# Kernel tuning notes

Measured on AMD Instinct MI355X. Metric: run time of the kernel, lower is better.

## Reference

```python
import math
import jax, jax.numpy as jnp
import numpy as np

B, N, E, H = 1, 4096, 256, 8
D = E // H  # head dim = 32


def setup_inputs() -> dict:
    key = jax.random.key(0)
    ks = jax.random.split(key, 10)
    s = 1.0 / math.sqrt(E)
    return {
        "x": jax.random.normal(ks[0], (B, N, E), dtype=jnp.float32),
        "adjacency": jax.random.randint(ks[1], (B, N, N), 0, 2, dtype=jnp.int32),
        "Wq": jax.random.normal(ks[2], (E, E), dtype=jnp.float32) * s,
        "bq": jnp.zeros((E,), dtype=jnp.float32),
        "Wk": jax.random.normal(ks[3], (E, E), dtype=jnp.float32) * s,
        "bk": jnp.zeros((E,), dtype=jnp.float32),
        "Wv": jax.random.normal(ks[4], (E, E), dtype=jnp.float32) * s,
        "bv": jnp.zeros((E,), dtype=jnp.float32),
        "Wo": jax.random.normal(ks[5], (E, E), dtype=jnp.float32) * s,
        "bo": jnp.zeros((E,), dtype=jnp.float32),
    }


def reference(x, adjacency, Wq, bq, Wk, bk, Wv, bv, Wo, bo):
    b, n, e = x.shape
    # projections (torch Linear: x @ W.T + b), split into heads -> [B,H,N,D]
    def heads(y):
        return y.reshape(b, n, H, D).transpose(0, 2, 1, 3)
    q = heads(x @ Wq.T + bq)
    k = heads(x @ Wk.T + bk)
    v = heads(x @ Wv.T + bv)
    scores = jnp.einsum("bhnd,bhmd->bhnm", q, k) / math.sqrt(D)
    mask = (adjacency[:, None, :, :] == 0)  # [B,1,N,N]
    scores = jnp.where(mask, -jnp.inf, scores)
    w = jax.nn.softmax(scores, axis=-1)
    out = jnp.einsum("bhnm,bhmd->bhnd", w, v)
    out = out.transpose(0, 2, 1, 3).reshape(b, n, e)
    return out @ Wo.T + bo
```

## Files before the change

### kernel.cpp

```cpp
#include <hip/hip_runtime.h>
#include <math.h>


#define NTOK 4096
#define EDIM 256
#define HEADS 8
#define HD 32
#define NSPLIT 2
#define QSCALE 0.17677669529663687f
#define LOG2E 1.4426950408889634f
#define CINIT (-11.541560327111707f)

typedef __attribute__((ext_vector_type(8))) short bf16x8;
typedef __attribute__((ext_vector_type(4))) float f32x4;
typedef __attribute__((ext_vector_type(4))) unsigned long long u64x4;

static __device__ inline short f2bf(float f) {
    unsigned u = __float_as_uint(f);
    u = (u + 0x7FFFu + ((u >> 16) & 1u)) >> 16;
    return (short)u;
}
static __device__ inline unsigned packtrunc(float a, float b) {
    return __builtin_amdgcn_perm(__float_as_uint(b), __float_as_uint(a),
                                 0x07060302u);
}
static __device__ inline float sel_mask(float v, unsigned long long m) {
    float r;
    asm("v_cndmask_b32 %0, 0, %1, %2" : "=v"(r) : "v"(v), "s"(m));
    return r;
}

__global__ __launch_bounds__(256) void prep(
    const int* __restrict__ adj, unsigned long long* __restrict__ maskT,
    const float* __restrict__ x,  const float* __restrict__ Wq,
    const float* __restrict__ Wk, const float* __restrict__ Wv,
    const float* __restrict__ Wo,
    short* __restrict__ xb,  short* __restrict__ wqb,
    short* __restrict__ wkb, short* __restrict__ wvb,
    short* __restrict__ wob)
{
    const int bid = blockIdx.x;
    if (bid < 16384) {
        const int w = bid * 4 + (threadIdx.x >> 6);
        const int l = threadIdx.x & 63;
        const int qb = w >> 8;
        const int kt = (w >> 2) & 63;
        const int b = w & 3;
        const int row = qb * 16 + (l & 15);
        const int col = kt * 64 + b * 16 + ((l >> 4) & 3) * 4;
        const int4 av = *(const int4*)&adj[row * NTOK + col];
        const unsigned long long m0 = __ballot(av.x != 0);
        const unsigned long long m1 = __ballot(av.y != 0);
        const unsigned long long m2 = __ballot(av.z != 0);
        const unsigned long long m3 = __ballot(av.w != 0);
        if (l == 0) {
            unsigned long long* dst = &maskT[(size_t)w * 4];
            dst[0] = m0; dst[1] = m1; dst[2] = m2; dst[3] = m3;
        }
    } else {
        const int gid = (bid - 16384) * 256 + threadIdx.x;
        const int e = gid * 4;
        const float* src; short* dst; int off;
        if (e < NTOK * EDIM) { src = x; dst = xb; off = e; }
        else {
            const int r = e - NTOK * EDIM;
            const int wsel = r >> 16;
            off = r & 65535;
            src = (wsel == 0) ? Wq : (wsel == 1) ? Wk : (wsel == 2) ? Wv : Wo;
            dst = (wsel == 0) ? wqb : (wsel == 1) ? wkb : (wsel == 2) ? wvb : wob;
        }
        float4 v = *(const float4*)&src[off];
        uint2 t;
        t.x = (unsigned short)f2bf(v.x) | ((unsigned)(unsigned short)f2bf(v.y) << 16);
        t.y = (unsigned short)f2bf(v.z) | ((unsigned)(unsigned short)f2bf(v.w) << 16);
        *(uint2*)&dst[off] = t;
    }
}

__global__ __launch_bounds__(256) void qkv_mfma(
    const short* __restrict__ xb,
    const short* __restrict__ Wqb, const short* __restrict__ Wkb,
    const short* __restrict__ Wvb,
    const float* __restrict__ bq, const float* __restrict__ bk,
    const float* __restrict__ bv,
    short* __restrict__ qo, short* __restrict__ ko, short* __restrict__ vto)
{
    const int tid = threadIdx.x;
    const int wv = tid >> 6, lane = tid & 63;
    const int grp = lane >> 4, lcol = lane & 15;
    const int wsel = blockIdx.y >> 2;
    const int n0 = (blockIdx.y & 3) << 6;
    const int m0 = blockIdx.x * 64 + wv * 16;
    const short* __restrict__ W = (wsel == 0) ? Wqb : (wsel == 1) ? Wkb : Wvb;
    const float* __restrict__ bias = (wsel == 0) ? bq : (wsel == 1) ? bk : bv;

    bf16x8 af[8];
#pragma unroll
    for (int k = 0; k < 8; ++k)
        af[k] = *(const bf16x8*)&xb[(m0 + lcol) * 256 + k * 32 + grp * 8];

    f32x4 acc[4] = {};
#pragma unroll
    for (int k = 0; k < 8; ++k) {
#pragma unroll
        for (int t = 0; t < 4; ++t) {
            const bf16x8 bt =
                *(const bf16x8*)&W[(n0 + t * 16 + lcol) * 256 + k * 32 + grp * 8];
            acc[t] = __builtin_amdgcn_mfma_f32_16x16x32_bf16(af[k], bt, acc[t], 0, 0, 0);
        }
    }
#pragma unroll
    for (int t = 0; t < 4; ++t) {
        const int feat = n0 + t * 16 + lcol;
        const float bval = bias[feat];
        const int h = feat >> 5, d = feat & 31;
        if (wsel == 2) {
            uint2 o;
            o.x = (unsigned short)f2bf(acc[t][0] + bval) |
                  ((unsigned)(unsigned short)f2bf(acc[t][1] + bval) << 16);
            o.y = (unsigned short)f2bf(acc[t][2] + bval) |
                  ((unsigned)(unsigned short)f2bf(acc[t][3] + bval) << 16);
            *(uint2*)&vto[h * (HD * NTOK) + d * NTOK + m0 + grp * 4] = o;
        } else {
            short* __restrict__ out = (wsel == 0) ? qo : ko;
            const float sc = (wsel == 0) ? (QSCALE * LOG2E) : 1.0f;
#pragma unroll
            for (int j = 0; j < 4; ++j)
                out[h * (NTOK * HD) + (m0 + grp * 4 + j) * HD + d] =
                    f2bf((acc[t][j] + bval) * sc);
        }
    }
}

__global__ __launch_bounds__(256) void attn_mfma(
    const short* __restrict__ qg, const short* __restrict__ kg,
    const short* __restrict__ vtg, const unsigned long long* __restrict__ maskT,
    float* __restrict__ o_part, float* __restrict__ l_part)
{
    const int h = blockIdx.y;
    const int split = blockIdx.z;
    const int q0 = blockIdx.x << 6;
    const short* __restrict__ Q  = qg  + h * (NTOK * HD);
    const short* __restrict__ K  = kg  + h * (NTOK * HD);
    const short* __restrict__ Vt = vtg + h * (HD * NTOK);

    __shared__ short Ks[2][64][40];
    __shared__ short Vs[2][32][72];
    __shared__ short P_lds[4][16][76];

    const int tid = threadIdx.x;
    const int wv = tid >> 6;
    const int lane = tid & 63;
    const int grp = lane >> 4;
    const int lcol = lane & 15;
    const int q0w = q0 + wv * 16;

    const int krow = tid >> 2, kc8 = (tid & 3) << 3;
    const int vrow = tid >> 3, vc8 = (tid & 7) << 3;

    const bf16x8 qfrag = *(const bf16x8*)&Q[(q0w + lcol) * HD + grp * 8];

    const int qb = __builtin_amdgcn_readfirstlane(blockIdx.x * 4 + wv);
    const unsigned long long* __restrict__ mbase = maskT + (size_t)qb * 1024;

    f32x4 ot[2] = {};
    float lsum = 0.f;

    const int kt_begin = split * (64 / NSPLIT);
    const int kt_end = kt_begin + (64 / NSPLIT);

    {
        const int k0 = kt_begin << 6;
        const int4 kr = *(const int4*)&K[(k0 + krow) * HD + kc8];
        const int4 vr = *(const int4*)&Vt[vrow * NTOK + k0 + vc8];
        *(int4*)&Ks[0][krow][kc8] = kr;
        *(int4*)&Vs[0][vrow][vc8] = vr;
    }
    __syncthreads();

    int cur = 0;
    for (int kt = kt_begin; kt < kt_end; ++kt) {
        int4 kr, vr;
        const bool has_next = (kt + 1 < kt_end);
        if (has_next) {
            const int k0n = (kt + 1) << 6;
            kr = *(const int4*)&K[(k0n + krow) * HD + kc8];
            vr = *(const int4*)&Vt[vrow * NTOK + k0n + vc8];
        }

        const u64x4* mp = (const u64x4*)(mbase + kt * 16);
        const u64x4 wa = mp[0], wb = mp[1], wc = mp[2], wd = mp[3];

        bf16x8 kf[4], vf[4];
#pragma unroll
        for (int b = 0; b < 4; ++b)
            kf[b] = *(const bf16x8*)&Ks[cur][b * 16 + lcol][grp * 8];
#pragma unroll
        for (int c = 0; c < 2; ++c) {
            vf[c * 2 + 0] = *(const bf16x8*)&Vs[cur][c * 16 + lcol][grp * 8];
            vf[c * 2 + 1] = *(const bf16x8*)&Vs[cur][c * 16 + lcol][32 + grp * 8];
        }

        f32x4 s[4];
#pragma unroll
        for (int b = 0; b < 4; ++b)
            s[b] = __builtin_amdgcn_mfma_f32_16x16x32_bf16(
                kf[b], qfrag, (f32x4){CINIT, CINIT, CINIT, CINIT}, 0, 0, 0);

#pragma unroll
        for (int b = 0; b < 4; ++b) {
            const u64x4 wj = (b == 0) ? wa : (b == 1) ? wb : (b == 2) ? wc : wd;
            const float p0 = sel_mask(__builtin_amdgcn_exp2f(s[b][0]), wj[0]);
            const float p1 = sel_mask(__builtin_amdgcn_exp2f(s[b][1]), wj[1]);
            const float p2 = sel_mask(__builtin_amdgcn_exp2f(s[b][2]), wj[2]);
            const float p3 = sel_mask(__builtin_amdgcn_exp2f(s[b][3]), wj[3]);
            lsum += (p0 + p1) + (p2 + p3);
            uint2 t;
            t.x = packtrunc(p0, p1);
            t.y = packtrunc(p2, p3);
            *(uint2*)&P_lds[wv][lcol][b * 16 + grp * 4] = t;
        }

        const uint2 pl0 = *(const uint2*)&P_lds[wv][lcol][grp * 8];
        const uint2 pl1 = *(const uint2*)&P_lds[wv][lcol][grp * 8 + 4];
        const uint2 pl2 = *(const uint2*)&P_lds[wv][lcol][32 + grp * 8];
        const uint2 pl3 = *(const uint2*)&P_lds[wv][lcol][32 + grp * 8 + 4];
        struct { uint2 a, b; } u0 = {pl0, pl1}, u1 = {pl2, pl3};
        const bf16x8 pf0 = __builtin_bit_cast(bf16x8, u0);
        const bf16x8 pf1 = __builtin_bit_cast(bf16x8, u1);

#pragma unroll
        for (int c = 0; c < 2; ++c) {
            ot[c] = __builtin_amdgcn_mfma_f32_16x16x32_bf16(vf[c * 2 + 0], pf0, ot[c], 0, 0, 0);
            ot[c] = __builtin_amdgcn_mfma_f32_16x16x32_bf16(vf[c * 2 + 1], pf1, ot[c], 0, 0, 0);
        }

        if (has_next) {
            *(int4*)&Ks[cur ^ 1][krow][kc8] = kr;
            *(int4*)&Vs[cur ^ 1][vrow][vc8] = vr;
        }
        __syncthreads();
        cur ^= 1;
    }

    lsum += __shfl_xor(lsum, 16);
    lsum += __shfl_xor(lsum, 32);

    float* __restrict__ ob = o_part + split * (NTOK * EDIM);
#pragma unroll
    for (int c = 0; c < 2; ++c) {
        float4 st;
        st.x = ot[c][0]; st.y = ot[c][1]; st.z = ot[c][2]; st.w = ot[c][3];
        *(float4*)&ob[(q0w + lcol) * EDIM + h * HD + c * 16 + grp * 4] = st;
    }
    if (grp == 0)
        l_part[split * (NTOK * HEADS) + (q0w + lcol) * HEADS + h] = lsum;
}

__global__ __launch_bounds__(256) void out_mfma(
    const float* __restrict__ o_part, const float* __restrict__ l_part,
    const short* __restrict__ Wob, const float* __restrict__ bo,
    float* __restrict__ Y)
{
    const int tid = threadIdx.x;
    const int wv = tid >> 6, lane = tid & 63;
    const int grp = lane >> 4, lcol = lane & 15;
    const int n0 = blockIdx.y << 6;
    const int m0 = blockIdx.x * 64 + wv * 16;
    const int r = m0 + lcol;

    bf16x8 af[8];
#pragma unroll
    for (int k = 0; k < 8; ++k) {
        float4 s0 = {0.f, 0.f, 0.f, 0.f}, s1 = {0.f, 0.f, 0.f, 0.f};
        float lv = 0.f;
#pragma unroll
        for (int s = 0; s < NSPLIT; ++s) {
            const float* op = &o_part[s * (NTOK * EDIM) + r * EDIM + k * 32 + grp * 8];
            const float4 t0 = *(const float4*)op;
            const float4 t1 = *(const float4*)(op + 4);
            s0.x += t0.x; s0.y += t0.y; s0.z += t0.z; s0.w += t0.w;
            s1.x += t1.x; s1.y += t1.y; s1.z += t1.z; s1.w += t1.w;
            lv += l_part[s * (NTOK * HEADS) + r * HEADS + k];
        }
        const float inv = 1.0f / lv;
        bf16x8 t;
        t[0] = f2bf(s0.x * inv); t[1] = f2bf(s0.y * inv);
        t[2] = f2bf(s0.z * inv); t[3] = f2bf(s0.w * inv);
        t[4] = f2bf(s1.x * inv); t[5] = f2bf(s1.y * inv);
        t[6] = f2bf(s1.z * inv); t[7] = f2bf(s1.w * inv);
        af[k] = t;
    }

    f32x4 acc[4] = {};
#pragma unroll
    for (int k = 0; k < 8; ++k) {
#pragma unroll
        for (int t = 0; t < 4; ++t) {
            const bf16x8 bt =
                *(const bf16x8*)&Wob[(n0 + t * 16 + lcol) * 256 + k * 32 + grp * 8];
            acc[t] = __builtin_amdgcn_mfma_f32_16x16x32_bf16(af[k], bt, acc[t], 0, 0, 0);
        }
    }
#pragma unroll
    for (int t = 0; t < 4; ++t) {
        const float bval = bo[n0 + t * 16 + lcol];
#pragma unroll
        for (int j = 0; j < 4; ++j)
            Y[(m0 + grp * 4 + j) * EDIM + n0 + t * 16 + lcol] = acc[t][j] + bval;
    }
}

extern "C" void kernel_launch(void* const* d_in, const int* in_sizes, int n_in,
                              void* d_out, int out_size, void* d_ws, size_t ws_size,
                              hipStream_t stream) {
    (void)in_sizes; (void)n_in; (void)out_size; (void)ws_size;
    const float* x  = (const float*)d_in[0];
    const int*  adj = (const int*)d_in[1];
    const float* Wq = (const float*)d_in[2];
    const float* bq = (const float*)d_in[3];
    const float* Wk = (const float*)d_in[4];
    const float* bk = (const float*)d_in[5];
    const float* Wv = (const float*)d_in[6];
    const float* bv = (const float*)d_in[7];
    const float* Wo = (const float*)d_in[8];
    const float* bo = (const float*)d_in[9];

    char* ws = (char*)d_ws;
    short* x_bf  = (short*)(ws);
    short* q_ws  = (short*)(ws + (2u << 20));
    short* k_ws  = (short*)(ws + (4u << 20));
    short* vt_ws = (short*)(ws + (6u << 20));
    unsigned long long* maskT =
        (unsigned long long*)(ws + (8u << 20));
    short* Wq_bf = (short*)(ws + (10u << 20));
    short* Wk_bf = Wq_bf + (EDIM * EDIM);
    short* Wv_bf = Wk_bf + (EDIM * EDIM);
    short* Wo_bf = Wv_bf + (EDIM * EDIM);
    float* l_part = (float*)(ws + (11u << 20));
    float* o_part = (float*)(ws + (12u << 20));

    prep<<<dim3(16384 + 1280), 256, 0, stream>>>(
        adj, maskT, x, Wq, Wk, Wv, Wo, x_bf, Wq_bf, Wk_bf, Wv_bf, Wo_bf);
    qkv_mfma<<<dim3(64, 12), 256, 0, stream>>>(x_bf, Wq_bf, Wk_bf, Wv_bf,
                                               bq, bk, bv, q_ws, k_ws, vt_ws);
    attn_mfma<<<dim3(64, HEADS, NSPLIT), 256, 0, stream>>>(
        q_ws, k_ws, vt_ws, maskT, o_part, l_part);
    out_mfma<<<dim3(64, 4), 256, 0, stream>>>(o_part, l_part, Wo_bf, bo,
                                              (float*)d_out);
}
```

Baseline: 179.3 us.

## Load K/V fragments directly from global into registers, compute row sums via MFMA

Removes the shared-memory K/V staging and per-tile __syncthreads, so each wave loads its MFMA fragments straight from global memory into registers with a two-tile register double buffer. The softmax denominator is now accumulated with extra MFMAs against a ones vector instead of scalar adds plus cross-lane shuffles. s_setprio hints are wrapped around the MFMA groups. In exchange, the four waves in a block now each fetch the same K/V data separately, relying on cache, and register pressure goes up.

```diff
diff --git a/kernel.cpp b/kernel.cpp
--- a/kernel.cpp
+++ b/kernel.cpp
@@ -144,8 +144,6 @@
     const short* __restrict__ K  = kg  + h * (NTOK * HD);
     const short* __restrict__ Vt = vtg + h * (HD * NTOK);
 
-    __shared__ short Ks[2][64][40];
-    __shared__ short Vs[2][32][72];
     __shared__ short P_lds[4][16][76];
 
     const int tid = threadIdx.x;
@@ -155,96 +153,90 @@
     const int lcol = lane & 15;
     const int q0w = q0 + wv * 16;
 
-    const int krow = tid >> 2, kc8 = (tid & 3) << 3;
-    const int vrow = tid >> 3, vc8 = (tid & 7) << 3;
-
     const bf16x8 qfrag = *(const bf16x8*)&Q[(q0w + lcol) * HD + grp * 8];
 
     const int qb = __builtin_amdgcn_readfirstlane(blockIdx.x * 4 + wv);
     const unsigned long long* __restrict__ mbase = maskT + (size_t)qb * 1024;
 
     f32x4 ot[2] = {};
-    float lsum = 0.f;
-
-    const int kt_begin = split * (64 / NSPLIT);
-    const int kt_end = kt_begin + (64 / NSPLIT);
-
-    {
-        const int k0 = kt_begin << 6;
-        const int4 kr = *(const int4*)&K[(k0 + krow) * HD + kc8];
-        const int4 vr = *(const int4*)&Vt[vrow * NTOK + k0 + vc8];
-        *(int4*)&Ks[0][krow][kc8] = kr;
-        *(int4*)&Vs[0][vrow][vc8] = vr;
-    }
-    __syncthreads();
-
-    int cur = 0;
-    for (int kt = kt_begin; kt < kt_end; ++kt) {
-        int4 kr, vr;
-        const bool has_next = (kt + 1 < kt_end);
-        if (has_next) {
-            const int k0n = (kt + 1) << 6;
-            kr = *(const int4*)&K[(k0n + krow) * HD + kc8];
-            vr = *(const int4*)&Vt[vrow * NTOK + k0n + vc8];
-        }
-
-        const u64x4* mp = (const u64x4*)(mbase + kt * 16);
-        const u64x4 wa = mp[0], wb = mp[1], wc = mp[2], wd = mp[3];
-
-        bf16x8 kf[4], vf[4];
-#pragma unroll
-        for (int b = 0; b < 4; ++b)
-            kf[b] = *(const bf16x8*)&Ks[cur][b * 16 + lcol][grp * 8];
-#pragma unroll
-        for (int c = 0; c < 2; ++c) {
-            vf[c * 2 + 0] = *(const bf16x8*)&Vs[cur][c * 16 + lcol][grp * 8];
-            vf[c * 2 + 1] = *(const bf16x8*)&Vs[cur][c * 16 + lcol][32 + grp * 8];
-        }
-
-        f32x4 s[4];
-#pragma unroll
-        for (int b = 0; b < 4; ++b)
-            s[b] = __builtin_amdgcn_mfma_f32_16x16x32_bf16(
-                kf[b], qfrag, (f32x4){CINIT, CINIT, CINIT, CINIT}, 0, 0, 0);
-
-#pragma unroll
-        for (int b = 0; b < 4; ++b) {
-            const u64x4 wj = (b == 0) ? wa : (b == 1) ? wb : (b == 2) ? wc : wd;
-            const float p0 = sel_mask(__builtin_amdgcn_exp2f(s[b][0]), wj[0]);
-            const float p1 = sel_mask(__builtin_amdgcn_exp2f(s[b][1]), wj[1]);
-            const float p2 = sel_mask(__builtin_amdgcn_exp2f(s[b][2]), wj[2]);
-            const float p3 = sel_mask(__builtin_amdgcn_exp2f(s[b][3]), wj[3]);
-            lsum += (p0 + p1) + (p2 + p3);
-            uint2 t;
-            t.x = packtrunc(p0, p1);
-            t.y = packtrunc(p2, p3);
-            *(uint2*)&P_lds[wv][lcol][b * 16 + grp * 4] = t;
-        }
-
-        const uint2 pl0 = *(const uint2*)&P_lds[wv][lcol][grp * 8];
-        const uint2 pl1 = *(const uint2*)&P_lds[wv][lcol][grp * 8 + 4];
-        const uint2 pl2 = *(const uint2*)&P_lds[wv][lcol][32 + grp * 8];
-        const uint2 pl3 = *(const uint2*)&P_lds[wv][lcol][32 + grp * 8 + 4];
-        struct { uint2 a, b; } u0 = {pl0, pl1}, u1 = {pl2, pl3};
-        const bf16x8 pf0 = __builtin_bit_cast(bf16x8, u0);
-        const bf16x8 pf1 = __builtin_bit_cast(bf16x8, u1);
-
-#pragma unroll
-        for (int c = 0; c < 2; ++c) {
-            ot[c] = __builtin_amdgcn_mfma_f32_16x16x32_bf16(vf[c * 2 + 0], pf0, ot[c], 0, 0, 0);
-            ot[c] = __builtin_amdgcn_mfma_f32_16x16x32_bf16(vf[c * 2 + 1], pf1, ot[c], 0, 0, 0);
-        }
-
-        if (has_next) {
-            *(int4*)&Ks[cur ^ 1][krow][kc8] = kr;
-            *(int4*)&Vs[cur ^ 1][vrow][vc8] = vr;
-        }
-        __syncthreads();
-        cur ^= 1;
-    }
-
-    lsum += __shfl_xor(lsum, 16);
-    lsum += __shfl_xor(lsum, 32);
+    f32x4 lacc = {};
+    const f32x4 cinit = {CINIT, CINIT, CINIT, CINIT};
+    bf16x8 ones;
+#pragma unroll
+    for (int i = 0; i < 8; ++i) ones[i] = (short)0x3F80;
+
+    const int NT = 64 / NSPLIT;
+    const int kt_begin = split * NT;
+
+    const short* __restrict__ kp = &K[(kt_begin * 64 + lcol) * HD + grp * 8];
+    const short* __restrict__ vp = &Vt[lcol * NTOK + kt_begin * 64 + grp * 8];
+
+#define LOADKV(KF, VF, T)                                                   \
+    {                                                                       \
+        const short* kpp = kp + (T) * (64 * HD);                            \
+        const short* vpp = vp + (T) * 64;                                   \
+        KF[0] = *(const bf16x8*)(kpp);                                      \
+        KF[1] = *(const bf16x8*)(kpp + 16 * HD);                            \
+        KF[2] = *(const bf16x8*)(kpp + 32 * HD);                            \
+        KF[3] = *(const bf16x8*)(kpp + 48 * HD);                            \
+        VF[0] = *(const bf16x8*)(vpp);                                      \
+        VF[1] = *(const bf16x8*)(vpp + 32);                                 \
+        VF[2] = *(const bf16x8*)(vpp + 16 * NTOK);                          \
+        VF[3] = *(const bf16x8*)(vpp + 16 * NTOK + 32);                     \
+    }
+
+#define TILE(KF, VF, KT)                                                    \
+    {                                                                       \
+        const u64x4* mp = (const u64x4*)(mbase + (size_t)(KT) * 16);        \
+        const u64x4 wa = mp[0], wb = mp[1], wcm = mp[2], wdm = mp[3];       \
+        f32x4 s[4];                                                         \
+        __builtin_amdgcn_s_setprio(1);                                      \
+        _Pragma("unroll")                                                   \
+        for (int b = 0; b < 4; ++b)                                         \
+            s[b] = __builtin_amdgcn_mfma_f32_16x16x32_bf16(                 \
+                KF[b], qfrag, cinit, 0, 0, 0);                              \
+        __builtin_amdgcn_s_setprio(0);                                      \
+        _Pragma("unroll")                                                   \
+        for (int b = 0; b < 4; ++b) {                                       \
+            const u64x4 wj = (b == 0) ? wa : (b == 1) ? wb                  \
+                             : (b == 2) ? wcm : wdm;                        \
+            const float p0 = sel_mask(__builtin_amdgcn_exp2f(s[b][0]), wj[0]); \
+            const float p1 = sel_mask(__builtin_amdgcn_exp2f(s[b][1]), wj[1]); \
+            const float p2 = sel_mask(__builtin_amdgcn_exp2f(s[b][2]), wj[2]); \
+            const float p3 = sel_mask(__builtin_amdgcn_exp2f(s[b][3]), wj[3]); \
+            uint2 t;                                                        \
+            t.x = packtrunc(p0, p1);                                        \
+            t.y = packtrunc(p2, p3);                                        \
+            *(uint2*)&P_lds[wv][lcol][b * 16 + grp * 4] = t;                \
+        }                                                                   \
+        const uint2 pl0 = *(const uint2*)&P_lds[wv][lcol][grp * 8];         \
+        const uint2 pl1 = *(const uint2*)&P_lds[wv][lcol][grp * 8 + 4];     \
+        const uint2 pl2 = *(const uint2*)&P_lds[wv][lcol][32 + grp * 8];    \
+        const uint2 pl3 = *(const uint2*)&P_lds[wv][lcol][32 + grp * 8 + 4];\
+        struct { uint2 a, b; } u0 = {pl0, pl1}, u1 = {pl2, pl3};            \
+        const bf16x8 pf0 = __builtin_bit_cast(bf16x8, u0);                  \
+        const bf16x8 pf1 = __builtin_bit_cast(bf16x8, u1);                  \
+        __builtin_amdgcn_s_setprio(1);                                      \
+        ot[0] = __builtin_amdgcn_mfma_f32_16x16x32_bf16(VF[0], pf0, ot[0], 0, 0, 0); \
+        ot[0] = __builtin_amdgcn_mfma_f32_16x16x32_bf16(VF[1], pf1, ot[0], 0, 0, 0); \
+        ot[1] = __builtin_amdgcn_mfma_f32_16x16x32_bf16(VF[2], pf0, ot[1], 0, 0, 0); \
+        ot[1] = __builtin_amdgcn_mfma_f32_16x16x32_bf16(VF[3], pf1, ot[1], 0, 0, 0); \
+        lacc  = __builtin_amdgcn_mfma_f32_16x16x32_bf16(ones,  pf0, lacc, 0, 0, 0);  \
+        lacc  = __builtin_amdgcn_mfma_f32_16x16x32_bf16(ones,  pf1, lacc, 0, 0, 0);  \
+        __builtin_amdgcn_s_setprio(0);                                      \
+    }
+
+    bf16x8 kA[4], vA[4], kB[4], vB[4];
+    LOADKV(kA, vA, 0)
+#pragma unroll 1
+    for (int t = 0; t < NT; t += 2) {
+        LOADKV(kB, vB, t + 1)
+        TILE(kA, vA, kt_begin + t)
+        if (t + 2 < NT) LOADKV(kA, vA, t + 2)
+        TILE(kB, vB, kt_begin + t + 1)
+    }
+#undef LOADKV
+#undef TILE
 
     float* __restrict__ ob = o_part + split * (NTOK * EDIM);
 #pragma unroll
@@ -254,7 +246,7 @@
         *(float4*)&ob[(q0w + lcol) * EDIM + h * HD + c * 16 + grp * 4] = st;
     }
     if (grp == 0)
-        l_part[split * (NTOK * HEADS) + (q0w + lcol) * HEADS + h] = lsum;
+        l_part[split * (NTOK * HEADS) + (q0w + lcol) * HEADS + h] = lacc[0];
 }
 
 __global__ __launch_bounds__(256) void out_mfma(
```

Result: slower. 226.2 us (+26.2%).

## Split attention over four key chunks, compute row sums via MFMA, regrid output GEMM

Applied to the files above, without the earlier changes.

The attention kernel now takes its key-split count from the grid (4 when the workspace is large enough, otherwise 2), doubling the number of blocks to improve occupancy across CUs. The softmax denominator is accumulated with an extra MFMA against a ones vector instead of scalar adds and shuffles, and MFMA sections get raised wave priority. The output projection is regridded so each wave computes one 16x16 tile, giving 4x more blocks, and it reduces a runtime number of partials. The cost is extra partial-buffer traffic and reduction work, plus the row sum now comes from bf16-truncated P.

```diff
diff --git a/kernel.cpp b/kernel.cpp
--- a/kernel.cpp
+++ b/kernel.cpp
@@ -6,7 +6,6 @@
 #define EDIM 256
 #define HEADS 8
 #define HD 32
-#define NSPLIT 2
 #define QSCALE 0.17677669529663687f
 #define LOG2E 1.4426950408889634f
 #define CINIT (-11.541560327111707f)
@@ -164,10 +163,15 @@
     const unsigned long long* __restrict__ mbase = maskT + (size_t)qb * 1024;
 
     f32x4 ot[2] = {};
-    float lsum = 0.f;
-
-    const int kt_begin = split * (64 / NSPLIT);
-    const int kt_end = kt_begin + (64 / NSPLIT);
+    f32x4 lacc = {};
+    const f32x4 cinit = {CINIT, CINIT, CINIT, CINIT};
+    bf16x8 ones;
+#pragma unroll
+    for (int i = 0; i < 8; ++i) ones[i] = (short)0x3F80;
+
+    const int tps = 64 / (int)gridDim.z;
+    const int kt_begin = split * tps;
+    const int kt_end = kt_begin + tps;
 
     {
         const int k0 = kt_begin << 6;
@@ -202,10 +206,12 @@
         }
 
         f32x4 s[4];
+        __builtin_amdgcn_s_setprio(1);
 #pragma unroll
         for (int b = 0; b < 4; ++b)
             s[b] = __builtin_amdgcn_mfma_f32_16x16x32_bf16(
-                kf[b], qfrag, (f32x4){CINIT, CINIT, CINIT, CINIT}, 0, 0, 0);
+                kf[b], qfrag, cinit, 0, 0, 0);
+        __builtin_amdgcn_s_setprio(0);
 
 #pragma unroll
         for (int b = 0; b < 4; ++b) {
@@ -214,7 +220,6 @@
             const float p1 = sel_mask(__builtin_amdgcn_exp2f(s[b][1]), wj[1]);
             const float p2 = sel_mask(__builtin_amdgcn_exp2f(s[b][2]), wj[2]);
             const float p3 = sel_mask(__builtin_amdgcn_exp2f(s[b][3]), wj[3]);
-            lsum += (p0 + p1) + (p2 + p3);
             uint2 t;
             t.x = packtrunc(p0, p1);
             t.y = packtrunc(p2, p3);
@@ -229,11 +234,15 @@
         const bf16x8 pf0 = __builtin_bit_cast(bf16x8, u0);
         const bf16x8 pf1 = __builtin_bit_cast(bf16x8, u1);
 
+        __builtin_amdgcn_s_setprio(1);
 #pragma unroll
         for (int c = 0; c < 2; ++c) {
             ot[c] = __builtin_amdgcn_mfma_f32_16x16x32_bf16(vf[c * 2 + 0], pf0, ot[c], 0, 0, 0);
             ot[c] = __builtin_amdgcn_mfma_f32_16x16x32_bf16(vf[c * 2 + 1], pf1, ot[c], 0, 0, 0);
         }
+        lacc = __builtin_amdgcn_mfma_f32_16x16x32_bf16(ones, pf0, lacc, 0, 0, 0);
+        lacc = __builtin_amdgcn_mfma_f32_16x16x32_bf16(ones, pf1, lacc, 0, 0, 0);
+        __builtin_amdgcn_s_setprio(0);
 
         if (has_next) {
             *(int4*)&Ks[cur ^ 1][krow][kc8] = kr;
@@ -242,9 +251,6 @@
         __syncthreads();
         cur ^= 1;
     }
-
-    lsum += __shfl_xor(lsum, 16);
-    lsum += __shfl_xor(lsum, 32);
 
     float* __restrict__ ob = o_part + split * (NTOK * EDIM);
 #pragma unroll
@@ -254,19 +260,19 @@
         *(float4*)&ob[(q0w + lcol) * EDIM + h * HD + c * 16 + grp * 4] = st;
     }
     if (grp == 0)
-        l_part[split * (NTOK * HEADS) + (q0w + lcol) * HEADS + h] = lsum;
+        l_part[split * (NTOK * HEADS) + (q0w + lcol) * HEADS + h] = lacc[0];
 }
 
 __global__ __launch_bounds__(256) void out_mfma(
     const float* __restrict__ o_part, const float* __restrict__ l_part,
     const short* __restrict__ Wob, const float* __restrict__ bo,
-    float* __restrict__ Y)
+    float* __restrict__ Y, int ns)
 {
     const int tid = threadIdx.x;
     const int wv = tid >> 6, lane = tid & 63;
     const int grp = lane >> 4, lcol = lane & 15;
-    const int n0 = blockIdx.y << 6;
-    const int m0 = blockIdx.x * 64 + wv * 16;
+    const int m0 = blockIdx.x << 4;
+    const int n0 = (blockIdx.y << 6) + wv * 16;
     const int r = m0 + lcol;
 
     bf16x8 af[8];
@@ -274,8 +280,7 @@
     for (int k = 0; k < 8; ++k) {
         float4 s0 = {0.f, 0.f, 0.f, 0.f}, s1 = {0.f, 0.f, 0.f, 0.f};
         float lv = 0.f;
-#pragma unroll
-        for (int s = 0; s < NSPLIT; ++s) {
+        for (int s = 0; s < ns; ++s) {
             const float* op = &o_part[s * (NTOK * EDIM) + r * EDIM + k * 32 + grp * 8];
             const float4 t0 = *(const float4*)op;
             const float4 t1 = *(const float4*)(op + 4);
@@ -292,29 +297,23 @@
         af[k] = t;
     }
 
-    f32x4 acc[4] = {};
+    f32x4 acc = {};
 #pragma unroll
     for (int k = 0; k < 8; ++k) {
-#pragma unroll
-        for (int t = 0; t < 4; ++t) {
-            const bf16x8 bt =
-                *(const bf16x8*)&Wob[(n0 + t * 16 + lcol) * 256 + k * 32 + grp * 8];
-            acc[t] = __builtin_amdgcn_mfma_f32_16x16x32_bf16(af[k], bt, acc[t], 0, 0, 0);
-        }
-    }
-#pragma unroll
-    for (int t = 0; t < 4; ++t) {
-        const float bval = bo[n0 + t * 16 + lcol];
-#pragma unroll
-        for (int j = 0; j < 4; ++j)
-            Y[(m0 + grp * 4 + j) * EDIM + n0 + t * 16 + lcol] = acc[t][j] + bval;
-    }
+        const bf16x8 bt =
+            *(const bf16x8*)&Wob[(n0 + lcol) * 256 + k * 32 + grp * 8];
+        acc = __builtin_amdgcn_mfma_f32_16x16x32_bf16(af[k], bt, acc, 0, 0, 0);
+    }
+    const float bval = bo[n0 + lcol];
+#pragma unroll
+    for (int j = 0; j < 4; ++j)
+        Y[(m0 + grp * 4 + j) * EDIM + n0 + lcol] = acc[j] + bval;
 }
 
 extern "C" void kernel_launch(void* const* d_in, const int* in_sizes, int n_in,
                               void* d_out, int out_size, void* d_ws, size_t ws_size,
                               hipStream_t stream) {
-    (void)in_sizes; (void)n_in; (void)out_size; (void)ws_size;
+    (void)in_sizes; (void)n_in; (void)out_size;
     const float* x  = (const float*)d_in[0];
     const int*  adj = (const int*)d_in[1];
     const float* Wq = (const float*)d_in[2];
@@ -340,12 +339,14 @@
     float* l_part = (float*)(ws + (11u << 20));
     float* o_part = (float*)(ws + (12u << 20));
 
+    const int ns = (ws_size >= (28u << 20)) ? 4 : 2;
+
     prep<<<dim3(16384 + 1280), 256, 0, stream>>>(
         adj, maskT, x, Wq, Wk, Wv, Wo, x_bf, Wq_bf, Wk_bf, Wv_bf, Wo_bf);
     qkv_mfma<<<dim3(64, 12), 256, 0, stream>>>(x_bf, Wq_bf, Wk_bf, Wv_bf,
                                                bq, bk, bv, q_ws, k_ws, vt_ws);
-    attn_mfma<<<dim3(64, HEADS, NSPLIT), 256, 0, stream>>>(
+    attn_mfma<<<dim3(64, HEADS, ns), 256, 0, stream>>>(
         q_ws, k_ws, vt_ws, maskT, o_part, l_part);
-    out_mfma<<<dim3(64, 4), 256, 0, stream>>>(o_part, l_part, Wo_bf, bo,
-                                              (float*)d_out);
-}
+    out_mfma<<<dim3(256, 4), 256, 0, stream>>>(o_part, l_part, Wo_bf, bo,
+                                               (float*)d_out, ns);
+}
```

Measured after the change: 215.4 us. 20.1% more time.
